# Kernel optimization log

Measured on AMD Instinct MI355X. Metric: run time of the kernel, lower is better.

Reference implementation:

```python
import jax, jax.numpy as jnp
import numpy as np

N_DRUG, N_MICROBE = 1500, 1572
N = N_DRUG + N_MICROBE          # 3072 nodes
F_IN = 1546                     # raw feature dim (fc1: 1546 -> 256)
D0 = 256                        # GCN input dim after fc1
H1 = H2 = 128                   # GCN hidden dims (H1 + H2 = 256)
B = 16384                       # number of (left,right) query pairs


def _sym_norm(A):
    # D^{-1/2} A D^{-1/2} (no self loops), zeros kept for isolated nodes
    deg = A.sum(axis=1)
    d = jnp.where(deg > 0, jax.lax.rsqrt(deg), 0.0)
    return A * d[:, None] * d[None, :]


def _compute_inf(adj, L):
    # dl.compute_inf: L-hop influence = L-th power of sym-normalized adjacency
    An = _sym_norm(adj)
    M = An
    for _ in range(L - 1):
        M = M @ An
    return M


def _gcn_norm(W):
    # GCNConv normalization: add self loops (weight 1), sym-normalize by weighted degree
    Ahat = W + jnp.eye(W.shape[0], dtype=W.dtype)
    deg = Ahat.sum(axis=1)
    d = jnp.where(deg > 0, jax.lax.rsqrt(deg), 0.0)
    return Ahat * d[:, None] * d[None, :]


def _glorot(key, shape):
    return jax.random.normal(key, shape, dtype=jnp.float32) / np.sqrt(shape[0])


def setup_inputs() -> dict:
    key = jax.random.key(0)
    ks = jax.random.split(key, 24)
    u = jax.random.uniform(ks[0], (N, N), dtype=jnp.float32)
    w = jax.random.uniform(ks[1], (N, N), dtype=jnp.float32)
    adj = jnp.where(u < 0.01, w, 0.0)
    adj = jnp.maximum(adj, adj.T)
    X = jax.random.normal(ks[2], (N, F_IN), dtype=jnp.float32)
    left = jax.random.randint(ks[3], (B,), 0, N)
    right = jax.random.randint(ks[4], (B,), 0, N)
    return dict(
        left=left, right=right, X=X, adj=adj, threshold=jnp.float32(1e-4),
        W_fc1=_glorot(ks[5], (F_IN, D0)), b_fc1=jnp.zeros((D0,), jnp.float32),
        Wg1=_glorot(ks[6], (D0, H1)), bg1=jnp.zeros((H1,), jnp.float32),
        Wg2=_glorot(ks[7], (H1, H2)), bg2=jnp.zeros((H2,), jnp.float32),
        Wg3=_glorot(ks[8], (D0, H1)), bg3=jnp.zeros((H1,), jnp.float32),
        Wg4=_glorot(ks[9], (H1, H2)), bg4=jnp.zeros((H2,), jnp.float32),
        Wg5=_glorot(ks[10], (D0, H1)), bg5=jnp.zeros((H1,), jnp.float32),
        Wg6=_glorot(ks[11], (H1, H2)), bg6=jnp.zeros((H2,), jnp.float32),
        cnn_k=jax.random.normal(ks[12], (1, 3, 3, 3), dtype=jnp.float32) * 0.1,
        cnn_b=jnp.zeros((1,), jnp.float32),
        W_a=_glorot(ks[13], (2 * (H1 + H2), 64)), b_a=jnp.zeros((64,), jnp.float32),
        W_b=_glorot(ks[14], (64, 2)), b_b=jnp.zeros((2,), jnp.float32),
    )


def reference(left, right, X, adj, threshold,
              W_fc1, b_fc1, Wg1, bg1, Wg2, bg2, Wg3, bg3, Wg4, bg4,
              Wg5, bg5, Wg6, bg6, cnn_k, cnn_b, W_a, b_a, W_b, b_b):
    X0 = jax.nn.relu(X @ W_fc1 + b_fc1)  # fc1: [N, 1546] -> [N, 256]

    def branch(mask_src, Wa, ba, Wb, bb):
        # dynamically thresholded edges carry the ORIGINAL adj weights
        Wadj = jnp.where(mask_src > threshold, adj, 0.0)
        An = _gcn_norm(Wadj)                       # [N, N]
        e1 = jax.nn.relu(An @ (X0 @ Wa) + ba)      # GCNConv 1
        e2 = jax.nn.relu(An @ (e1 @ Wb) + bb)      # GCNConv 2
        return jnp.concatenate([e1, e2], axis=1)   # [N, 256]

    emb_l2 = branch(_compute_inf(adj, 2), Wg1, bg1, Wg2, bg2)
    emb_l1 = branch(_compute_inf(adj, 1), Wg3, bg3, Wg4, bg4)
    emb_l0 = branch(adj, Wg5, bg5, Wg6, bg6)

    emb = jnp.stack([emb_l0, emb_l1, emb_l2], axis=0)[None]  # [1, 3, N, 256]
    conv = jax.lax.conv_general_dilated(
        emb, cnn_k, window_strides=(1, 1), padding=[(2, 2), (2, 2)],
        rhs_dilation=(2, 2), dimension_numbers=('NCHW', 'OIHW', 'NCHW'))
    emb_all = conv[0, 0] + cnn_b[0]                # [N, 256]

    pair = jnp.concatenate([emb_all[left], emb_all[right]], axis=1)  # [B, 512]
    h = jax.nn.relu(pair @ W_a + b_a)              # dropout is identity at eval
    logits = h @ W_b + b_b                         # [B, 2]
    return logits, emb_all
```

## Files before the change

kernel.cpp:

```cpp
#include <hip/hip_runtime.h>

#define NN 3072
#define FIN 1546
#define KP 1568
#define MAXR 192
#define KSPLIT 7
#define KSLICE 224

#define XS4_BLOCKS (NN * KP / 1024)
#define WSPLIT_BLOCKS (256 * KP / 256)
#define CSR_BLOCKS (NN / 4)

typedef __attribute__((ext_vector_type(8))) __bf16 bf16x8;
typedef __attribute__((ext_vector_type(4))) __bf16 bf16x4;
typedef __attribute__((ext_vector_type(4))) float f32x4;

__global__ __launch_bounds__(256) void prep_k(const float* __restrict__ adj,
                                              int* __restrict__ cols, float* __restrict__ vals,
                                              int* __restrict__ cnt, float* __restrict__ dvec,
                                              const float* __restrict__ X,
                                              __bf16* __restrict__ Xh, __bf16* __restrict__ Xl,
                                              const float* __restrict__ W,
                                              __bf16* __restrict__ WhT, __bf16* __restrict__ WlT) {
    int bid = blockIdx.x;
    if (bid < XS4_BLOCKS) {
        int e = (bid * 256 + threadIdx.x) * 4;
        int i = e / KP, c = e - i * KP;
        const float* xr = X + (size_t)i * FIN + c;
        float x0 = (c + 0 < FIN) ? xr[0] : 0.f;
        float x1 = (c + 1 < FIN) ? xr[1] : 0.f;
        float x2 = (c + 2 < FIN) ? xr[2] : 0.f;
        float x3 = (c + 3 < FIN) ? xr[3] : 0.f;
        __bf16 h0 = (__bf16)x0, h1 = (__bf16)x1, h2 = (__bf16)x2, h3 = (__bf16)x3;
        bf16x4 hv = {h0, h1, h2, h3};
        bf16x4 lv = {(__bf16)(x0 - (float)h0), (__bf16)(x1 - (float)h1),
                     (__bf16)(x2 - (float)h2), (__bf16)(x3 - (float)h3)};
        *(bf16x4*)(Xh + e) = hv;
        *(bf16x4*)(Xl + e) = lv;
        return;
    }
    bid -= XS4_BLOCKS;
    if (bid < WSPLIT_BLOCKS) {
        int idx = bid * 256 + threadIdx.x;
        int c = idx / KP, k = idx - c * KP;
        float x = (k < FIN) ? W[(size_t)k * 256 + c] : 0.f;
        __bf16 h = (__bf16)x;
        WhT[idx] = h;
        WlT[idx] = (__bf16)(x - (float)h);
        return;
    }
    bid -= WSPLIT_BLOCKS;
    int i = bid * 4 + (threadIdx.x >> 6);
    int lane = threadIdx.x & 63;
    const float* row = adj + (size_t)i * NN;
    unsigned long long below = (1ull << lane) - 1ull;
    float s = 0.f; int count = 0;
    int base = i * MAXR;
    for (int c0 = 0; c0 < NN; c0 += 256) {
        float4 a4 = *(const float4*)(row + c0 + lane * 4);
        float a[4] = {a4.x, a4.y, a4.z, a4.w};
        s += a[0] + a[1] + a[2] + a[3];
        unsigned long long bal[4];
        #pragma unroll
        for (int u = 0; u < 4; u++) bal[u] = __ballot(a[u] != 0.f);
        int before = 0;
        #pragma unroll
        for (int u = 0; u < 4; u++) before += __popcll(bal[u] & below);
        int local = 0;
        #pragma unroll
        for (int u = 0; u < 4; u++) {
            if (a[u] != 0.f) {
                int pos = count + before + local;
                if (pos < MAXR) { cols[base + pos] = c0 + lane * 4 + u; vals[base + pos] = a[u]; }
                local++;
            }
        }
        int tot = 0;
        #pragma unroll
        for (int u = 0; u < 4; u++) tot += __popcll(bal[u]);
        count += tot;
    }
    for (int off = 32; off; off >>= 1) s += __shfl_xor(s, off);
    if (lane == 0) {
        cnt[i] = count < MAXR ? count : MAXR;
        dvec[i] = (s > 0.f) ? 1.0f / sqrtf(s) : 0.f;
    }
}

__global__ __launch_bounds__(256) void fc1m_k(const __bf16* __restrict__ Xh,
                                              const __bf16* __restrict__ Xl,
                                              const __bf16* __restrict__ WhT,
                                              const __bf16* __restrict__ WlT,
                                              float* __restrict__ Cpart) {
    int tid = threadIdx.x;
    int w = tid >> 6, lane = tid & 63;
    int m = lane & 15, q = lane >> 4;
    int i0 = blockIdx.x * 64, c0 = blockIdx.y * 64;
    int z = blockIdx.z;
    int k0 = z * KSLICE;
    int rowA = i0 + w * 16 + m;
    const __bf16* xh = Xh + (size_t)rowA * KP + k0 + q * 8;
    const __bf16* xl = Xl + (size_t)rowA * KP + k0 + q * 8;
    const __bf16* bh0 = WhT + (size_t)(c0 + m) * KP + k0 + q * 8;
    const __bf16* bl0 = WlT + (size_t)(c0 + m) * KP + k0 + q * 8;

    f32x4 acc[4];
    #pragma unroll
    for (int ct = 0; ct < 4; ct++)
        #pragma unroll
        for (int r = 0; r < 4; r++) acc[ct][r] = 0.f;

    for (int ks = 0; ks < KSLICE; ks += 32) {
        bf16x8 ah = *(const bf16x8*)(xh + ks);
        bf16x8 al = *(const bf16x8*)(xl + ks);
        #pragma unroll
        for (int ct = 0; ct < 4; ct++) {
            bf16x8 bh = *(const bf16x8*)(bh0 + (size_t)ct * 16 * KP + ks);
            bf16x8 bl = *(const bf16x8*)(bl0 + (size_t)ct * 16 * KP + ks);
            acc[ct] = __builtin_amdgcn_mfma_f32_16x16x32_bf16(ah, bh, acc[ct], 0, 0, 0);
            acc[ct] = __builtin_amdgcn_mfma_f32_16x16x32_bf16(ah, bl, acc[ct], 0, 0, 0);
            acc[ct] = __builtin_amdgcn_mfma_f32_16x16x32_bf16(al, bh, acc[ct], 0, 0, 0);
        }
    }
    float* outp = Cpart + (size_t)z * NN * 256;
    int rowBase = i0 + w * 16 + q * 4;
    #pragma unroll
    for (int ct = 0; ct < 4; ct++) {
        int col = c0 + ct * 16 + m;
        #pragma unroll
        for (int r = 0; r < 4; r++)
            outp[(size_t)(rowBase + r) * 256 + col] = acc[ct][r];
    }
}

__global__ __launch_bounds__(256) void maskall_k(const int* __restrict__ cols,
                                                 const float* __restrict__ vals,
                                                 const int* __restrict__ cnt,
                                                 const float* __restrict__ dvec,
                                                 const float* __restrict__ thrp,
                                                 int* __restrict__ mcols,
                                                 float* __restrict__ mvals,
                                                 int* __restrict__ mcnt,
                                                 float* __restrict__ db,
                                                 const float* __restrict__ Cpart,
                                                 const float* __restrict__ bias,
                                                 float* __restrict__ X0) {
    __shared__ float ds[NN];
    __shared__ int lcols[MAXR];
    __shared__ float lvals[MAXR];
    __shared__ int lcnt;
    __shared__ float osum;
    int i = blockIdx.x, tid = threadIdx.x, mode = blockIdx.y;

    if (mode == 3) {
        if (tid < 64) {
            int idx4 = i * 64 + tid;
            int c4 = tid << 2;
            float4 s = ((const float4*)Cpart)[idx4];
            #pragma unroll
            for (int z = 1; z < KSPLIT; z++) {
                float4 t = ((const float4*)(Cpart + (size_t)z * NN * 256))[idx4];
                s.x += t.x; s.y += t.y; s.z += t.z; s.w += t.w;
            }
            float4 b = *(const float4*)&bias[c4];
            s.x = fmaxf(s.x + b.x, 0.f); s.y = fmaxf(s.y + b.y, 0.f);
            s.z = fmaxf(s.z + b.z, 0.f); s.w = fmaxf(s.w + b.w, 0.f);
            ((float4*)X0)[idx4] = s;
        }
        return;
    }

    mcols += (size_t)mode * NN * MAXR;
    mvals += (size_t)mode * NN * MAXR;
    mcnt  += (size_t)mode * NN;
    db    += (size_t)mode * NN;
    int ni = cnt[i], base = i * MAXR;
    float thr = *thrp;
    float di = dvec[i];

    if (mode < 2) {
        if (tid == 0) lcnt = 0;
        __syncthreads();
        float s = 0.f;
        if (tid < ni) {
            int j = cols[base + tid];
            float a = vals[base + tid];
            float m = (mode == 0) ? a : a * di * dvec[j];
            if (m > thr) {
                int p = atomicAdd(&lcnt, 1);
                mcols[base + p] = j;
                mvals[base + p] = a;
                s = a;
            }
        }
        ds[tid] = s; __syncthreads();
        for (int off = 128; off; off >>= 1) {
            if (tid < off) ds[tid] += ds[tid + off];
            __syncthreads();
        }
        if (tid == 0) {
            mcnt[i] = lcnt;
            db[i] = 1.0f / sqrtf(ds[0] + 1.0f);
        }
        return;
    }

    if (tid == 0) { osum = 0.f; lcnt = 0; }
    for (int j = tid; j < NN; j += 256) ds[j] = 0.f;
    __syncthreads();
    for (int t = tid; t < ni; t += 256) {
        int j = cols[base + t];
        float a = vals[base + t];
        lcols[t] = j; lvals[t] = a;
        ds[j] = a * dvec[j] * dvec[j];
    }
    __syncthreads();
    int lane = tid & 63, wv = tid >> 6;
    int sub = lane & 15, dg = lane >> 4;
    for (int o = wv * 4 + dg; o < ni; o += 16) {
        int j = lcols[o];
        int nj = cnt[j], bj = j * MAXR;
        float dot = 0.f;
        for (int t = sub; t < nj; t += 16)
            dot += vals[bj + t] * ds[cols[bj + t]];
        #pragma unroll
        for (int off = 8; off; off >>= 1) dot += __shfl_xor(dot, off);
        if (sub == 0 && di * dvec[j] * dot > thr) {
            int p = atomicAdd(&lcnt, 1);
            mcols[base + p] = j;
            mvals[base + p] = lvals[o];
            atomicAdd(&osum, lvals[o]);
        }
    }
    __syncthreads();
    if (tid == 0) {
        mcnt[i] = lcnt;
        db[i] = 1.0f / sqrtf(osum + 1.0f);
    }
}

__global__ __launch_bounds__(256) void gemm3_k(const float* __restrict__ A, int aplane, int lda,
                                               const float* __restrict__ B0,
                                               const float* __restrict__ B1,
                                               const float* __restrict__ B2,
                                               int K, float* __restrict__ out) {
    __shared__ float Ast[16][68];
    __shared__ float Bs[16][64];
    int tid = threadIdx.x;
    int tx = tid & 15, ty = tid >> 4;
    int i0 = blockIdx.x * 64, c0 = blockIdx.y * 64;
    int z = blockIdx.z;
    const float* Ab = A + (size_t)z * aplane;
    const float* B = (z == 0) ? B0 : (z == 1) ? B1 : B2;
    float* outp = out + (size_t)z * NN * 128;
    int sr = tid >> 4, sk = tid & 15;
    int bk = tid >> 4, bc4 = (tid & 15) << 2;

    float ap[4]; float4 bp;
    #pragma unroll
    for (int u = 0; u < 4; u++) ap[u] = Ab[(size_t)(i0 + sr + u * 16) * lda + sk];
    bp = *(const float4*)&B[(size_t)bk * 128 + c0 + bc4];

    float acc[4][4];
    #pragma unroll
    for (int r = 0; r < 4; r++)
        #pragma unroll
        for (int c = 0; c < 4; c++) acc[r][c] = 0.f;

    for (int kt = 0; kt < K; kt += 16) {
        __syncthreads();
        #pragma unroll
        for (int u = 0; u < 4; u++) Ast[sk][sr + u * 16] = ap[u];
        *(float4*)&Bs[bk][bc4] = bp;
        __syncthreads();
        int kn = kt + 16;
        if (kn < K) {
            #pragma unroll
            for (int u = 0; u < 4; u++) ap[u] = Ab[(size_t)(i0 + sr + u * 16) * lda + kn + sk];
            bp = *(const float4*)&B[(size_t)(kn + bk) * 128 + c0 + bc4];
        }
        #pragma unroll
        for (int kk = 0; kk < 16; kk++) {
            float4 a = *(const float4*)&Ast[kk][ty * 4];
            float4 b = *(const float4*)&Bs[kk][tx * 4];
            const float* av = (const float*)&a;
            const float* bv = (const float*)&b;
            #pragma unroll
            for (int r = 0; r < 4; r++)
                #pragma unroll
                for (int c = 0; c < 4; c++) acc[r][c] += av[r] * bv[c];
        }
    }
    #pragma unroll
    for (int r = 0; r < 4; r++) {
        int row = i0 + ty * 4 + r;
        float4 v = make_float4(acc[r][0], acc[r][1], acc[r][2], acc[r][3]);
        *(float4*)&outp[(size_t)row * 128 + c0 + tx * 4] = v;
    }
}

__global__ __launch_bounds__(256) void spmm3_k(const int* __restrict__ mcols,
                                               const float* __restrict__ mvals,
                                               const int* __restrict__ mcnt,
                                               const float* __restrict__ db,
                                               const float* __restrict__ Xin,
                                               const float* __restrict__ bias0,
                                               const float* __restrict__ bias1,
                                               const float* __restrict__ bias2,
                                               float* __restrict__ outA,
                                               float* __restrict__ embf, int coff) {
    __shared__ float lcoef[MAXR];
    __shared__ int lj[MAXR];
    __shared__ float4 part[8][32];
    int i = blockIdx.x, tid = threadIdx.x, b = blockIdx.y;
    mcols += (size_t)b * NN * MAXR;
    mvals += (size_t)b * NN * MAXR;
    mcnt  += (size_t)b * NN;
    db    += (size_t)b * NN;
    const float* Xb = Xin + (size_t)b * NN * 128;
    const float* bias = (b == 0) ? bias0 : (b == 1) ? bias1 : bias2;
    float dbi = db[i];
    int n = mcnt[i], base = i * MAXR;
    if (tid < n) {
        int j = mcols[base + tid];
        lj[tid] = j;
        lcoef[tid] = mvals[base + tid] * dbi * db[j];
    }
    __syncthreads();
    int g = tid >> 5, c4 = (tid & 31) << 2;
    float4 acc = make_float4(0.f, 0.f, 0.f, 0.f);
    if (g == 0) {
        float4 x = *(const float4*)&Xb[(size_t)i * 128 + c4];
        float d2 = dbi * dbi;
        acc = make_float4(d2 * x.x, d2 * x.y, d2 * x.z, d2 * x.w);
    }
    for (int t = g; t < n; t += 8) {
        float cf = lcoef[t];
        float4 x = *(const float4*)&Xb[(size_t)lj[t] * 128 + c4];
        acc.x += cf * x.x; acc.y += cf * x.y; acc.z += cf * x.z; acc.w += cf * x.w;
    }
    part[g][tid & 31] = acc;
    __syncthreads();
    if (tid < 32) {
        float4 s = part[0][tid];
        #pragma unroll
        for (int gg = 1; gg < 8; gg++) {
            float4 t4 = part[gg][tid];
            s.x += t4.x; s.y += t4.y; s.z += t4.z; s.w += t4.w;
        }
        int cc = tid << 2;
        float4 bv = *(const float4*)&bias[cc];
        s.x = fmaxf(s.x + bv.x, 0.f); s.y = fmaxf(s.y + bv.y, 0.f);
        s.z = fmaxf(s.z + bv.z, 0.f); s.w = fmaxf(s.w + bv.w, 0.f);
        if (outA) *(float4*)&outA[((size_t)b * NN + i) * 128 + cc] = s;
        *(float4*)&embf[((size_t)b * NN + i) * 256 + coff + cc] = s;
    }
}

__global__ __launch_bounds__(256) void conv3f_k(const float* __restrict__ emb,
                                                const float* __restrict__ ck,
                                                const float* __restrict__ cb,
                                                float* __restrict__ outf) {
    __shared__ float rows[3][3][256];
    int n = blockIdx.x, c = threadIdx.x;
    #pragma unroll
    for (int i = 0; i < 3; i++)
        #pragma unroll
        for (int kh = 0; kh < 3; kh++) {
            int nn2 = n + 2 * kh - 2;
            rows[i][kh][c] = (nn2 >= 0 && nn2 < NN) ? emb[((size_t)i * NN + nn2) * 256 + c] : 0.f;
        }
    __syncthreads();
    float s = cb[0];
    #pragma unroll
    for (int i = 0; i < 3; i++)
        #pragma unroll
        for (int kh = 0; kh < 3; kh++)
            #pragma unroll
            for (int kw = 0; kw < 3; kw++) {
                int cc = c + 2 * kw - 2;
                if (cc >= 0 && cc < 256)
                    s += rows[i][kh][cc] * ck[(i * 3 + kh) * 3 + kw];
            }
    outf[(size_t)n * 256 + c] = s;
}

__global__ __launch_bounds__(256) void gemmUV_k(const float* __restrict__ A,
                                                const float* __restrict__ Wa,
                                                float* __restrict__ uvp) {
    __shared__ float Ast[16][68];
    __shared__ float Bs[16][64];
    int tid = threadIdx.x;
    int tx = tid & 15, ty = tid >> 4;
    int i0 = blockIdx.x * 64;
    int half = blockIdx.y;
    int z = blockIdx.z;
    int ks = z * 128;
    const float* Bb = Wa + (half ? 256 * 64 : 0);
    int sr = tid >> 4, sk = tid & 15;
    int bk = tid >> 4, bc4 = (tid & 15) << 2;

    float ap[4]; float4 bp;
    #pragma unroll
    for (int u = 0; u < 4; u++) ap[u] = A[(size_t)(i0 + sr + u * 16) * 256 + ks + sk];
    bp = *(const float4*)&Bb[(size_t)(ks + bk) * 64 + bc4];

    float acc[4][4];
    #pragma unroll
    for (int r = 0; r < 4; r++)
        #pragma unroll
        for (int c = 0; c < 4; c++) acc[r][c] = 0.f;

    for (int kt = ks; kt < ks + 128; kt += 16) {
        __syncthreads();
        #pragma unroll
        for (int u = 0; u < 4; u++) Ast[sk][sr + u * 16] = ap[u];
        *(float4*)&Bs[bk][bc4] = bp;
        __syncthreads();
        int kn = kt + 16;
        if (kn < ks + 128) {
            #pragma unroll
            for (int u = 0; u < 4; u++) ap[u] = A[(size_t)(i0 + sr + u * 16) * 256 + kn + sk];
            bp = *(const float4*)&Bb[(size_t)(kn + bk) * 64 + bc4];
        }
        #pragma unroll
        for (int kk = 0; kk < 16; kk++) {
            float4 a = *(const float4*)&Ast[kk][ty * 4];
            float4 b = *(const float4*)&Bs[kk][tx * 4];
            const float* av = (const float*)&a;
            const float* bv = (const float*)&b;
            #pragma unroll
            for (int r = 0; r < 4; r++)
                #pragma unroll
                for (int c = 0; c < 4; c++) acc[r][c] += av[r] * bv[c];
        }
    }
    float* outp = uvp + (size_t)z * NN * 128;
    #pragma unroll
    for (int r = 0; r < 4; r++) {
        int row = i0 + ty * 4 + r;
        float4 v = make_float4(acc[r][0], acc[r][1], acc[r][2], acc[r][3]);
        *(float4*)&outp[(size_t)row * 128 + half * 64 + tx * 4] = v;
    }
}

__global__ __launch_bounds__(256) void pairuv_k(const int* __restrict__ left,
                                                const int* __restrict__ right,
                                                const float* __restrict__ uvp,
                                                const float* __restrict__ ba,
                                                const float* __restrict__ Wb,
                                                const float* __restrict__ bb,
                                                float* __restrict__ out) {
    int tid = threadIdx.x;
    int w = tid >> 6, c = tid & 63;
    int base = blockIdx.x * 16 + w * 4;
    const float* u0 = uvp;
    const float* u1 = uvp + (size_t)NN * 128;
    float bac = ba[c];
    float w0 = Wb[c * 2], w1 = Wb[c * 2 + 1];
    float b0 = bb[0], b1 = bb[1];
    #pragma unroll
    for (int pp = 0; pp < 4; pp++) {
        int row = base + pp;
        int l = left[row], r = right[row];
        float h = u0[(size_t)l * 128 + c] + u1[(size_t)l * 128 + c]
                + u0[(size_t)r * 128 + 64 + c] + u1[(size_t)r * 128 + 64 + c] + bac;
        h = fmaxf(h, 0.f);
        float s0 = h * w0, s1 = h * w1;
        for (int off = 32; off; off >>= 1) {
            s0 += __shfl_xor(s0, off);
            s1 += __shfl_xor(s1, off);
        }
        if (c == 0) {
            out[row * 2]     = s0 + b0;
            out[row * 2 + 1] = s1 + b1;
        }
    }
}

extern "C" void kernel_launch(void* const* d_in, const int* in_sizes, int n_in,
                              void* d_out, int out_size, void* d_ws, size_t ws_size,
                              hipStream_t stream) {
    const int* left  = (const int*)d_in[0];
    const int* right = (const int*)d_in[1];
    const float* X    = (const float*)d_in[2];
    const float* adj  = (const float*)d_in[3];
    const float* thr  = (const float*)d_in[4];
    const float* Wfc1 = (const float*)d_in[5];
    const float* bfc1 = (const float*)d_in[6];
    const float* Wga[3] = { (const float*)d_in[15], (const float*)d_in[11], (const float*)d_in[7] };
    const float* bga[3] = { (const float*)d_in[16], (const float*)d_in[12], (const float*)d_in[8] };
    const float* Wgb[3] = { (const float*)d_in[17], (const float*)d_in[13], (const float*)d_in[9] };
    const float* bgb[3] = { (const float*)d_in[18], (const float*)d_in[14], (const float*)d_in[10] };
    const float* cnnk = (const float*)d_in[19];
    const float* cnnb = (const float*)d_in[20];
    const float* Wa_  = (const float*)d_in[21];
    const float* ba_  = (const float*)d_in[22];
    const float* Wb_  = (const float*)d_in[23];
    const float* bb_  = (const float*)d_in[24];

    char* p = (char*)d_ws;
    auto take = [&](size_t n) { char* q = p; p += (n + 255) & ~(size_t)255; return q; };
    float* dvec = (float*)take(NN * 4);
    float* db3  = (float*)take((size_t)3 * NN * 4);
    int*   cnt  = (int*)take(NN * 4);
    int*   mcnt3 = (int*)take((size_t)3 * NN * 4);
    int*   cols = (int*)take((size_t)NN * MAXR * 4);
    float* vals = (float*)take((size_t)NN * MAXR * 4);
    int*   mcols3 = (int*)take((size_t)3 * NN * MAXR * 4);
    float* mvals3 = (float*)take((size_t)3 * NN * MAXR * 4);
    float* X0    = (float*)take((size_t)NN * 256 * 4);
    float* XWall = (float*)take((size_t)3 * NN * 128 * 4);
    float* e1all = (float*)take((size_t)3 * NN * 128 * 4);
    float* HW2all= (float*)take((size_t)3 * NN * 128 * 4);
    float* embf  = (float*)take((size_t)3 * NN * 256 * 4);
    __bf16* Xl   = (__bf16*)take((size_t)NN * KP * 2);
    __bf16* WhT  = (__bf16*)take((size_t)256 * KP * 2);
    __bf16* WlT  = (__bf16*)take((size_t)256 * KP * 2);
    __bf16* Xh = (__bf16*)mcols3;
    float* Cpart = XWall;
    float* uvp = embf;

    float* out_logits = (float*)d_out;
    float* out_emb = out_logits + 32768;

    prep_k<<<XS4_BLOCKS + WSPLIT_BLOCKS + CSR_BLOCKS, 256, 0, stream>>>(
        adj, cols, vals, cnt, dvec, X, Xh, Xl, Wfc1, WhT, WlT);

    fc1m_k<<<dim3(NN / 64, 4, KSPLIT), 256, 0, stream>>>(Xh, Xl, WhT, WlT, Cpart);

    maskall_k<<<dim3(NN, 4), 256, 0, stream>>>(cols, vals, cnt, dvec, thr,
                                               mcols3, mvals3, mcnt3, db3,
                                               Cpart, bfc1, X0);

    gemm3_k<<<dim3(NN / 64, 2, 3), 256, 0, stream>>>(X0, 0, 256, Wga[0], Wga[1], Wga[2], 256, XWall);
    spmm3_k<<<dim3(NN, 3), 256, 0, stream>>>(mcols3, mvals3, mcnt3, db3, XWall,
                                             bga[0], bga[1], bga[2], e1all, embf, 0);
    gemm3_k<<<dim3(NN / 64, 2, 3), 256, 0, stream>>>(e1all, NN * 128, 128, Wgb[0], Wgb[1], Wgb[2], 128, HW2all);
    spmm3_k<<<dim3(NN, 3), 256, 0, stream>>>(mcols3, mvals3, mcnt3, db3, HW2all,
                                             bgb[0], bgb[1], bgb[2], (float*)0, embf, 128);

    conv3f_k<<<NN, 256, 0, stream>>>(embf, cnnk, cnnb, out_emb);
    gemmUV_k<<<dim3(NN / 64, 2, 2), 256, 0, stream>>>(out_emb, Wa_, uvp);
    pairuv_k<<<16384 / 16, 256, 0, stream>>>(left, right, uvp, ba_, Wb_, bb_, out_logits);
}
```

Baseline: 304.0 us.

## Move GCN and pair-projection GEMMs to split-bf16 MFMA

```diff
diff --git a/kernel.cpp b/kernel.cpp
--- a/kernel.cpp
+++ b/kernel.cpp
@@ -9,6 +9,7 @@
 
 #define XS4_BLOCKS (NN * KP / 1024)
 #define WSPLIT_BLOCKS (256 * KP / 256)
+#define WG_BLOCKS 704
 #define CSR_BLOCKS (NN / 4)
 
 typedef __attribute__((ext_vector_type(8))) __bf16 bf16x8;
@@ -21,7 +22,17 @@
                                               const float* __restrict__ X,
                                               __bf16* __restrict__ Xh, __bf16* __restrict__ Xl,
                                               const float* __restrict__ W,
-                                              __bf16* __restrict__ WhT, __bf16* __restrict__ WlT) {
+                                              __bf16* __restrict__ WhT, __bf16* __restrict__ WlT,
+                                              const float* __restrict__ Wga0,
+                                              const float* __restrict__ Wga1,
+                                              const float* __restrict__ Wga2,
+                                              const float* __restrict__ Wgb0,
+                                              const float* __restrict__ Wgb1,
+                                              const float* __restrict__ Wgb2,
+                                              const float* __restrict__ Wa,
+                                              __bf16* __restrict__ WgaTh, __bf16* __restrict__ WgaTl,
+                                              __bf16* __restrict__ WgbTh, __bf16* __restrict__ WgbTl,
+                                              __bf16* __restrict__ WaTh, __bf16* __restrict__ WaTl) {
     int bid = blockIdx.x;
     if (bid < XS4_BLOCKS) {
         int e = (bid * 256 + threadIdx.x) * 4;
@@ -50,6 +61,36 @@
         return;
     }
     bid -= WSPLIT_BLOCKS;
+    if (bid < WG_BLOCKS) {
+        int idx = bid * 256 + threadIdx.x;
+        float x;
+        __bf16 *oh, *ol;
+        int off;
+        if (idx < 98304) {
+            int b = idx >> 15, r = idx & 32767;
+            int c = r >> 8, k = r & 255;
+            const float* Wp = (b == 0) ? Wga0 : (b == 1) ? Wga1 : Wga2;
+            x = Wp[k * 128 + c];
+            oh = WgaTh; ol = WgaTl; off = idx;
+        } else if (idx < 98304 + 49152) {
+            int j = idx - 98304;
+            int b = j >> 14, r = j & 16383;
+            int c = r >> 7, k = r & 127;
+            const float* Wp = (b == 0) ? Wgb0 : (b == 1) ? Wgb1 : Wgb2;
+            x = Wp[k * 128 + c];
+            oh = WgbTh; ol = WgbTl; off = j;
+        } else {
+            int j = idx - 147456;
+            int c = j >> 8, k = j & 255;
+            x = (c < 64) ? Wa[(size_t)k * 64 + c] : Wa[(size_t)(256 + k) * 64 + (c - 64)];
+            oh = WaTh; ol = WaTl; off = j;
+        }
+        __bf16 h = (__bf16)x;
+        oh[off] = h;
+        ol[off] = (__bf16)(x - (float)h);
+        return;
+    }
+    bid -= WG_BLOCKS;
     int i = bid * 4 + (threadIdx.x >> 6);
     int lane = threadIdx.x & 63;
     const float* row = adj + (size_t)i * NN;
@@ -144,7 +185,8 @@
                                                  float* __restrict__ db,
                                                  const float* __restrict__ Cpart,
                                                  const float* __restrict__ bias,
-                                                 float* __restrict__ X0) {
+                                                 __bf16* __restrict__ X0h,
+                                                 __bf16* __restrict__ X0l) {
     __shared__ float ds[NN];
     __shared__ int lcols[MAXR];
     __shared__ float lvals[MAXR];
@@ -165,7 +207,12 @@
             float4 b = *(const float4*)&bias[c4];
             s.x = fmaxf(s.x + b.x, 0.f); s.y = fmaxf(s.y + b.y, 0.f);
             s.z = fmaxf(s.z + b.z, 0.f); s.w = fmaxf(s.w + b.w, 0.f);
-            ((float4*)X0)[idx4] = s;
+            __bf16 h0 = (__bf16)s.x, h1 = (__bf16)s.y, h2 = (__bf16)s.z, h3 = (__bf16)s.w;
+            bf16x4 hv = {h0, h1, h2, h3};
+            bf16x4 lv = {(__bf16)(s.x - (float)h0), (__bf16)(s.y - (float)h1),
+                         (__bf16)(s.z - (float)h2), (__bf16)(s.w - (float)h3)};
+            *(bf16x4*)(X0h + (size_t)i * 256 + c4) = hv;
+            *(bf16x4*)(X0l + (size_t)i * 256 + c4) = lv;
         }
         return;
     }
@@ -239,63 +286,49 @@
     }
 }
 
-__global__ __launch_bounds__(256) void gemm3_k(const float* __restrict__ A, int aplane, int lda,
-                                               const float* __restrict__ B0,
-                                               const float* __restrict__ B1,
-                                               const float* __restrict__ B2,
-                                               int K, float* __restrict__ out) {
-    __shared__ float Ast[16][68];
-    __shared__ float Bs[16][64];
+__global__ __launch_bounds__(256) void gemm3m_k(const __bf16* __restrict__ Ah,
+                                                const __bf16* __restrict__ Al,
+                                                int aplane, int K,
+                                                const __bf16* __restrict__ Bh,
+                                                const __bf16* __restrict__ Bl,
+                                                float* __restrict__ out) {
     int tid = threadIdx.x;
-    int tx = tid & 15, ty = tid >> 4;
+    int w = tid >> 6, lane = tid & 63;
+    int m = lane & 15, q = lane >> 4;
     int i0 = blockIdx.x * 64, c0 = blockIdx.y * 64;
     int z = blockIdx.z;
-    const float* Ab = A + (size_t)z * aplane;
-    const float* B = (z == 0) ? B0 : (z == 1) ? B1 : B2;
+    int rowA = i0 + w * 16 + m;
+    const __bf16* ah = Ah + (size_t)z * aplane + (size_t)rowA * K + q * 8;
+    const __bf16* al = Al + (size_t)z * aplane + (size_t)rowA * K + q * 8;
+    const __bf16* bh0 = Bh + (size_t)z * 128 * K + (size_t)(c0 + m) * K + q * 8;
+    const __bf16* bl0 = Bl + (size_t)z * 128 * K + (size_t)(c0 + m) * K + q * 8;
+
+    f32x4 acc[4];
+    #pragma unroll
+    for (int ct = 0; ct < 4; ct++)
+        #pragma unroll
+        for (int r = 0; r < 4; r++) acc[ct][r] = 0.f;
+
+    for (int ks = 0; ks < K; ks += 32) {
+        bf16x8 a_h = *(const bf16x8*)(ah + ks);
+        bf16x8 a_l = *(const bf16x8*)(al + ks);
+        #pragma unroll
+        for (int ct = 0; ct < 4; ct++) {
+            bf16x8 b_h = *(const bf16x8*)(bh0 + (size_t)ct * 16 * K + ks);
+            bf16x8 b_l = *(const bf16x8*)(bl0 + (size_t)ct * 16 * K + ks);
+            acc[ct] = __builtin_amdgcn_mfma_f32_16x16x32_bf16(a_h, b_h, acc[ct], 0, 0, 0);
+            acc[ct] = __builtin_amdgcn_mfma_f32_16x16x32_bf16(a_h, b_l, acc[ct], 0, 0, 0);
+            acc[ct] = __builtin_amdgcn_mfma_f32_16x16x32_bf16(a_l, b_h, acc[ct], 0, 0, 0);
+        }
+    }
     float* outp = out + (size_t)z * NN * 128;
-    int sr = tid >> 4, sk = tid & 15;
-    int bk = tid >> 4, bc4 = (tid & 15) << 2;
-
-    float ap[4]; float4 bp;
-    #pragma unroll
-    for (int u = 0; u < 4; u++) ap[u] = Ab[(size_t)(i0 + sr + u * 16) * lda + sk];
-    bp = *(const float4*)&B[(size_t)bk * 128 + c0 + bc4];
-
-    float acc[4][4];
-    #pragma unroll
-    for (int r = 0; r < 4; r++)
-        #pragma unroll
-        for (int c = 0; c < 4; c++) acc[r][c] = 0.f;
-
-    for (int kt = 0; kt < K; kt += 16) {
-        __syncthreads();
-        #pragma unroll
-        for (int u = 0; u < 4; u++) Ast[sk][sr + u * 16] = ap[u];
-        *(float4*)&Bs[bk][bc4] = bp;
-        __syncthreads();
-        int kn = kt + 16;
-        if (kn < K) {
-            #pragma unroll
-            for (int u = 0; u < 4; u++) ap[u] = Ab[(size_t)(i0 + sr + u * 16) * lda + kn + sk];
-            bp = *(const float4*)&B[(size_t)(kn + bk) * 128 + c0 + bc4];
-        }
-        #pragma unroll
-        for (int kk = 0; kk < 16; kk++) {
-            float4 a = *(const float4*)&Ast[kk][ty * 4];
-            float4 b = *(const float4*)&Bs[kk][tx * 4];
-            const float* av = (const float*)&a;
-            const float* bv = (const float*)&b;
-            #pragma unroll
-            for (int r = 0; r < 4; r++)
-                #pragma unroll
-                for (int c = 0; c < 4; c++) acc[r][c] += av[r] * bv[c];
-        }
-    }
-    #pragma unroll
-    for (int r = 0; r < 4; r++) {
-        int row = i0 + ty * 4 + r;
-        float4 v = make_float4(acc[r][0], acc[r][1], acc[r][2], acc[r][3]);
-        *(float4*)&outp[(size_t)row * 128 + c0 + tx * 4] = v;
+    int rowBase = i0 + w * 16 + q * 4;
+    #pragma unroll
+    for (int ct = 0; ct < 4; ct++) {
+        int col = c0 + ct * 16 + m;
+        #pragma unroll
+        for (int r = 0; r < 4; r++)
+            outp[(size_t)(rowBase + r) * 128 + col] = acc[ct][r];
     }
 }
 
@@ -307,7 +340,8 @@
                                                const float* __restrict__ bias0,
                                                const float* __restrict__ bias1,
                                                const float* __restrict__ bias2,
-                                               float* __restrict__ outA,
+                                               __bf16* __restrict__ outAh,
+                                               __bf16* __restrict__ outAl,
                                                float* __restrict__ embf, int coff) {
     __shared__ float lcoef[MAXR];
     __shared__ int lj[MAXR];
@@ -329,16 +363,27 @@
     __syncthreads();
     int g = tid >> 5, c4 = (tid & 31) << 2;
     float4 acc = make_float4(0.f, 0.f, 0.f, 0.f);
+    float4 acc2 = make_float4(0.f, 0.f, 0.f, 0.f);
     if (g == 0) {
         float4 x = *(const float4*)&Xb[(size_t)i * 128 + c4];
         float d2 = dbi * dbi;
         acc = make_float4(d2 * x.x, d2 * x.y, d2 * x.z, d2 * x.w);
     }
-    for (int t = g; t < n; t += 8) {
+    int t = g;
+    for (; t + 8 < n; t += 16) {
+        float cf0 = lcoef[t];
+        float4 x0 = *(const float4*)&Xb[(size_t)lj[t] * 128 + c4];
+        float cf1 = lcoef[t + 8];
+        float4 x1 = *(const float4*)&Xb[(size_t)lj[t + 8] * 128 + c4];
+        acc.x += cf0 * x0.x; acc.y += cf0 * x0.y; acc.z += cf0 * x0.z; acc.w += cf0 * x0.w;
+        acc2.x += cf1 * x1.x; acc2.y += cf1 * x1.y; acc2.z += cf1 * x1.z; acc2.w += cf1 * x1.w;
+    }
+    if (t < n) {
         float cf = lcoef[t];
         float4 x = *(const float4*)&Xb[(size_t)lj[t] * 128 + c4];
         acc.x += cf * x.x; acc.y += cf * x.y; acc.z += cf * x.z; acc.w += cf * x.w;
     }
+    acc.x += acc2.x; acc.y += acc2.y; acc.z += acc2.z; acc.w += acc2.w;
     part[g][tid & 31] = acc;
     __syncthreads();
     if (tid < 32) {
@@ -352,7 +397,14 @@
         float4 bv = *(const float4*)&bias[cc];
         s.x = fmaxf(s.x + bv.x, 0.f); s.y = fmaxf(s.y + bv.y, 0.f);
         s.z = fmaxf(s.z + bv.z, 0.f); s.w = fmaxf(s.w + bv.w, 0.f);
-        if (outA) *(float4*)&outA[((size_t)b * NN + i) * 128 + cc] = s;
+        if (outAh) {
+            __bf16 h0 = (__bf16)s.x, h1 = (__bf16)s.y, h2 = (__bf16)s.z, h3 = (__bf16)s.w;
+            bf16x4 hv = {h0, h1, h2, h3};
+            bf16x4 lv = {(__bf16)(s.x - (float)h0), (__bf16)(s.y - (float)h1),
+                         (__bf16)(s.z - (float)h2), (__bf16)(s.w - (float)h3)};
+            *(bf16x4*)(outAh + ((size_t)b * NN + i) * 128 + cc) = hv;
+            *(bf16x4*)(outAl + ((size_t)b * NN + i) * 128 + cc) = lv;
+        }
         *(float4*)&embf[((size_t)b * NN + i) * 256 + coff + cc] = s;
     }
 }
@@ -360,7 +412,9 @@
 __global__ __launch_bounds__(256) void conv3f_k(const float* __restrict__ emb,
                                                 const float* __restrict__ ck,
                                                 const float* __restrict__ cb,
-                                                float* __restrict__ outf) {
+                                                float* __restrict__ outf,
+                                                __bf16* __restrict__ embh,
+                                                __bf16* __restrict__ embl) {
     __shared__ float rows[3][3][256];
     int n = blockIdx.x, c = threadIdx.x;
     #pragma unroll
@@ -382,65 +436,56 @@
                 if (cc >= 0 && cc < 256)
                     s += rows[i][kh][cc] * ck[(i * 3 + kh) * 3 + kw];
             }
-    outf[(size_t)n * 256 + c] = s;
-}
-
-__global__ __launch_bounds__(256) void gemmUV_k(const float* __restrict__ A,
-                                                const float* __restrict__ Wa,
-                                                float* __restrict__ uvp) {
-    __shared__ float Ast[16][68];
-    __shared__ float Bs[16][64];
+    size_t idx = (size_t)n * 256 + c;
+    outf[idx] = s;
+    __bf16 h = (__bf16)s;
+    embh[idx] = h;
+    embl[idx] = (__bf16)(s - (float)h);
+}
+
+__global__ __launch_bounds__(256) void gemmuvm_k(const __bf16* __restrict__ Ah,
+                                                 const __bf16* __restrict__ Al,
+                                                 const __bf16* __restrict__ Bh,
+                                                 const __bf16* __restrict__ Bl,
+                                                 float* __restrict__ uvp) {
     int tid = threadIdx.x;
-    int tx = tid & 15, ty = tid >> 4;
-    int i0 = blockIdx.x * 64;
-    int half = blockIdx.y;
+    int w = tid >> 6, lane = tid & 63;
+    int m = lane & 15, q = lane >> 4;
+    int i0 = blockIdx.x * 64, c0 = blockIdx.y * 64;
     int z = blockIdx.z;
-    int ks = z * 128;
-    const float* Bb = Wa + (half ? 256 * 64 : 0);
-    int sr = tid >> 4, sk = tid & 15;
-    int bk = tid >> 4, bc4 = (tid & 15) << 2;
-
-    float ap[4]; float4 bp;
-    #pragma unroll
-    for (int u = 0; u < 4; u++) ap[u] = A[(size_t)(i0 + sr + u * 16) * 256 + ks + sk];
-    bp = *(const float4*)&Bb[(size_t)(ks + bk) * 64 + bc4];
-
-    float acc[4][4];
-    #pragma unroll
-    for (int r = 0; r < 4; r++)
-        #pragma unroll
-        for (int c = 0; c < 4; c++) acc[r][c] = 0.f;
-
-    for (int kt = ks; kt < ks + 128; kt += 16) {
-        __syncthreads();
-        #pragma unroll
-        for (int u = 0; u < 4; u++) Ast[sk][sr + u * 16] = ap[u];
-        *(float4*)&Bs[bk][bc4] = bp;
-        __syncthreads();
-        int kn = kt + 16;
-        if (kn < ks + 128) {
-            #pragma unroll
-            for (int u = 0; u < 4; u++) ap[u] = A[(size_t)(i0 + sr + u * 16) * 256 + kn + sk];
-            bp = *(const float4*)&Bb[(size_t)(kn + bk) * 64 + bc4];
-        }
-        #pragma unroll
-        for (int kk = 0; kk < 16; kk++) {
-            float4 a = *(const float4*)&Ast[kk][ty * 4];
-            float4 b = *(const float4*)&Bs[kk][tx * 4];
-            const float* av = (const float*)&a;
-            const float* bv = (const float*)&b;
-            #pragma unroll
-            for (int r = 0; r < 4; r++)
-                #pragma unroll
-                for (int c = 0; c < 4; c++) acc[r][c] += av[r] * bv[c];
+    int k0 = z * 128;
+    int rowA = i0 + w * 16 + m;
+    const __bf16* ah = Ah + (size_t)rowA * 256 + k0 + q * 8;
+    const __bf16* al = Al + (size_t)rowA * 256 + k0 + q * 8;
+    const __bf16* bh0 = Bh + (size_t)(c0 + m) * 256 + k0 + q * 8;
+    const __bf16* bl0 = Bl + (size_t)(c0 + m) * 256 + k0 + q * 8;
+
+    f32x4 acc[4];
+    #pragma unroll
+    for (int ct = 0; ct < 4; ct++)
+        #pragma unroll
+        for (int r = 0; r < 4; r++) acc[ct][r] = 0.f;
+
+    for (int ks = 0; ks < 128; ks += 32) {
+        bf16x8 a_h = *(const bf16x8*)(ah + ks);
+        bf16x8 a_l = *(const bf16x8*)(al + ks);
+        #pragma unroll
+        for (int ct = 0; ct < 4; ct++) {
+            bf16x8 b_h = *(const bf16x8*)(bh0 + (size_t)ct * 16 * 256 + ks);
+            bf16x8 b_l = *(const bf16x8*)(bl0 + (size_t)ct * 16 * 256 + ks);
+            acc[ct] = __builtin_amdgcn_mfma_f32_16x16x32_bf16(a_h, b_h, acc[ct], 0, 0, 0);
+            acc[ct] = __builtin_amdgcn_mfma_f32_16x16x32_bf16(a_h, b_l, acc[ct], 0, 0, 0);
+            acc[ct] = __builtin_amdgcn_mfma_f32_16x16x32_bf16(a_l, b_h, acc[ct], 0, 0, 0);
         }
     }
     float* outp = uvp + (size_t)z * NN * 128;
-    #pragma unroll
-    for (int r = 0; r < 4; r++) {
-        int row = i0 + ty * 4 + r;
-        float4 v = make_float4(acc[r][0], acc[r][1], acc[r][2], acc[r][3]);
-        *(float4*)&outp[(size_t)row * 128 + half * 64 + tx * 4] = v;
+    int rowBase = i0 + w * 16 + q * 4;
+    #pragma unroll
+    for (int ct = 0; ct < 4; ct++) {
+        int col = c0 + ct * 16 + m;
+        #pragma unroll
+        for (int r = 0; r < 4; r++)
+            outp[(size_t)(rowBase + r) * 128 + col] = acc[ct][r];
     }
 }
 
@@ -509,14 +554,24 @@
     float* vals = (float*)take((size_t)NN * MAXR * 4);
     int*   mcols3 = (int*)take((size_t)3 * NN * MAXR * 4);
     float* mvals3 = (float*)take((size_t)3 * NN * MAXR * 4);
-    float* X0    = (float*)take((size_t)NN * 256 * 4);
+    __bf16* X0h  = (__bf16*)take((size_t)NN * 256 * 2);
+    __bf16* X0l  = (__bf16*)take((size_t)NN * 256 * 2);
     float* XWall = (float*)take((size_t)3 * NN * 128 * 4);
-    float* e1all = (float*)take((size_t)3 * NN * 128 * 4);
+    __bf16* e1h  = (__bf16*)take((size_t)3 * NN * 128 * 2);
+    __bf16* e1l  = (__bf16*)take((size_t)3 * NN * 128 * 2);
     float* HW2all= (float*)take((size_t)3 * NN * 128 * 4);
     float* embf  = (float*)take((size_t)3 * NN * 256 * 4);
     __bf16* Xl   = (__bf16*)take((size_t)NN * KP * 2);
     __bf16* WhT  = (__bf16*)take((size_t)256 * KP * 2);
     __bf16* WlT  = (__bf16*)take((size_t)256 * KP * 2);
+    __bf16* WgaTh = (__bf16*)take((size_t)3 * 128 * 256 * 2);
+    __bf16* WgaTl = (__bf16*)take((size_t)3 * 128 * 256 * 2);
+    __bf16* WgbTh = (__bf16*)take((size_t)3 * 128 * 128 * 2);
+    __bf16* WgbTl = (__bf16*)take((size_t)3 * 128 * 128 * 2);
+    __bf16* WaTh  = (__bf16*)take((size_t)128 * 256 * 2);
+    __bf16* WaTl  = (__bf16*)take((size_t)128 * 256 * 2);
+    __bf16* embh  = (__bf16*)take((size_t)NN * 256 * 2);
+    __bf16* embl  = (__bf16*)take((size_t)NN * 256 * 2);
     __bf16* Xh = (__bf16*)mcols3;
     float* Cpart = XWall;
     float* uvp = embf;
@@ -524,23 +579,25 @@
     float* out_logits = (float*)d_out;
     float* out_emb = out_logits + 32768;
 
-    prep_k<<<XS4_BLOCKS + WSPLIT_BLOCKS + CSR_BLOCKS, 256, 0, stream>>>(
-        adj, cols, vals, cnt, dvec, X, Xh, Xl, Wfc1, WhT, WlT);
+    prep_k<<<XS4_BLOCKS + WSPLIT_BLOCKS + WG_BLOCKS + CSR_BLOCKS, 256, 0, stream>>>(
+        adj, cols, vals, cnt, dvec, X, Xh, Xl, Wfc1, WhT, WlT,
+        Wga[0], Wga[1], Wga[2], Wgb[0], Wgb[1], Wgb[2], Wa_,
+        WgaTh, WgaTl, WgbTh, WgbTl, WaTh, WaTl);
 
     fc1m_k<<<dim3(NN / 64, 4, KSPLIT), 256, 0, stream>>>(Xh, Xl, WhT, WlT, Cpart);
 
     maskall_k<<<dim3(NN, 4), 256, 0, stream>>>(cols, vals, cnt, dvec, thr,
                                                mcols3, mvals3, mcnt3, db3,
-                                               Cpart, bfc1, X0);
-
-    gemm3_k<<<dim3(NN / 64, 2, 3), 256, 0, stream>>>(X0, 0, 256, Wga[0], Wga[1], Wga[2], 256, XWall);
+                                               Cpart, bfc1, X0h, X0l);
+
+    gemm3m_k<<<dim3(NN / 64, 2, 3), 256, 0, stream>>>(X0h, X0l, 0, 256, WgaTh, WgaTl, XWall);
     spmm3_k<<<dim3(NN, 3), 256, 0, stream>>>(mcols3, mvals3, mcnt3, db3, XWall,
-                                             bga[0], bga[1], bga[2], e1all, embf, 0);
-    gemm3_k<<<dim3(NN / 64, 2, 3), 256, 0, stream>>>(e1all, NN * 128, 128, Wgb[0], Wgb[1], Wgb[2], 128, HW2all);
+                                             bga[0], bga[1], bga[2], e1h, e1l, embf, 0);
+    gemm3m_k<<<dim3(NN / 64, 2, 3), 256, 0, stream>>>(e1h, e1l, NN * 128, 128, WgbTh, WgbTl, HW2all);
     spmm3_k<<<dim3(NN, 3), 256, 0, stream>>>(mcols3, mvals3, mcnt3, db3, HW2all,
-                                             bgb[0], bgb[1], bgb[2], (float*)0, embf, 128);
-
-    conv3f_k<<<NN, 256, 0, stream>>>(embf, cnnk, cnnb, out_emb);
-    gemmUV_k<<<dim3(NN / 64, 2, 2), 256, 0, stream>>>(out_emb, Wa_, uvp);
+                                             bgb[0], bgb[1], bgb[2], (__bf16*)0, (__bf16*)0, embf, 128);
+
+    conv3f_k<<<NN, 256, 0, stream>>>(embf, cnnk, cnnb, out_emb, embh, embl);
+    gemmuvm_k<<<dim3(NN / 64, 2, 2), 256, 0, stream>>>(embh, embl, WaTh, WaTl, uvp);
     pairuv_k<<<16384 / 16, 256, 0, stream>>>(left, right, uvp, ba_, Wb_, bb_, out_logits);
 }
```

Measured after the change: 307.9 us. About the same (+1.3%).
